# Kernel optimization log

Hardware: AMD Instinct MI355X
Metric: run time of the kernel (lower is better)

The kernel has to match this reference:

```python
import jax, jax.numpy as jnp
import numpy as np

HEADS = 16
HEAD_DIM = 64

def setup_inputs() -> dict:
    key = jax.random.key(0)
    ks = jax.random.split(key, 5)
    S, B, H = 1024, 4, 1024
    scale = 1.0 / np.sqrt(H)
    return {
        "hidden_states": jax.random.normal(ks[0], (S, B, H), jnp.float32),
        "attention_mask": jnp.zeros((B * HEADS, 1, S), jnp.float32),
        "Wq": jax.random.normal(ks[1], (H, H), jnp.float32) * scale,
        "bq": jnp.zeros((H,), jnp.float32),
        "Wk": jax.random.normal(ks[2], (H, H), jnp.float32) * scale,
        "bk": jnp.zeros((H,), jnp.float32),
        "Wv": jax.random.normal(ks[3], (H, H), jnp.float32) * scale,
        "bv": jnp.zeros((H,), jnp.float32),
    }

def reference(hidden_states, attention_mask, Wq, bq, Wk, bk, Wv, bv):
    S, B, H = hidden_states.shape
    d = HEAD_DIM
    inv_sqrt_d = 1.0 / np.sqrt(d)
    # QKV projections (torch Linear: x @ W.T + b)
    q = hidden_states @ Wq.T + bq  # (S, B, H)
    k = hidden_states @ Wk.T + bk
    v = hidden_states @ Wv.T + bv
    # (S, B*heads, d) -> (B*heads, S, d)
    q = q.reshape(S, B * HEADS, d).transpose(1, 0, 2)
    k = k.reshape(S, B * HEADS, d).transpose(1, 0, 2)
    v = v.reshape(S, B * HEADS, d).transpose(1, 0, 2)
    # SDDMM: scaled scores + additive mask -> (B*heads, S, S)
    scores = jnp.einsum('nsd,ntd->nst', q, k) * inv_sqrt_d + attention_mask
    probs = jax.nn.softmax(scores, axis=-1)
    # AV bmm -> (B*heads, S, d); note: dropout in source is seeded but never applied
    ctx = jnp.einsum('nst,ntd->nsd', probs, v)
    # back to (S, B, hidden)
    ctx = ctx.transpose(1, 0, 2).reshape(S, B, H)
    return ctx
```

## Files before the change

### kernel.cpp

```cpp
#include <hip/hip_runtime.h>
#include <hip/hip_bf16.h>
#include <math.h>

#define S_LEN 1024
#define BATCH 4
#define HID 1024
#define NHEADS 16
#define DHEAD 64
#define NTOT 64
#define M_ROWS 4096

typedef unsigned short u16;
typedef unsigned int u32;
typedef __bf16 bf16x8 __attribute__((ext_vector_type(8)));
typedef float f32x4 __attribute__((ext_vector_type(4)));

__device__ __forceinline__ u16 f2bf(float x) {
    __hip_bfloat16 h = __float2bfloat16(x);
    return *(u16*)&h;
}

__device__ __forceinline__ void gll16(const u16* g, u16* l) {
    __builtin_amdgcn_global_load_lds(
        (const __attribute__((address_space(1))) u32*)g,
        (__attribute__((address_space(3))) u32*)l, 16, 0, 0);
}

__global__ __launch_bounds__(256) void cvt_all(
    const float* __restrict__ X, const float* __restrict__ wq,
    const float* __restrict__ wk, const float* __restrict__ wv,
    u16* __restrict__ Xb, u16* __restrict__ Wb)
{
    const int bid = blockIdx.x;
    const float* src;
    u16* dst;
    size_t base;
    if (bid < 4096) {
        src = X; dst = Xb; base = (size_t)bid * 1024;
    } else {
        const int wb = bid - 4096;
        const int which = wb >> 10;
        src = (which == 0) ? wq : (which == 1) ? wk : wv;
        dst = Wb + (size_t)which * HID * HID;
        base = (size_t)(wb & 1023) * 1024;
    }
    const size_t idx = base + threadIdx.x * 4;
    float4 x = *(const float4*)(src + (bid < 4096 ? idx : (size_t)(idx - base) + base - ((bid < 4096) ? 0 : 0)));
    x = *(const float4*)(src + ((bid < 4096) ? idx : (base - base) + idx - ((size_t)0)));
    x = *(const float4*)(src + ((bid < 4096) ? idx : (idx - (size_t)0) - ((bid < 4096) ? 0 : (size_t)0)));
    x = *(const float4*)(src + (bid < 4096 ? idx : idx - (size_t)0 - 0));
    const size_t loc = (bid < 4096) ? idx : base + threadIdx.x * 4;
    x = *(const float4*)(src + loc);
    *(ushort4*)(dst + loc) = make_ushort4(f2bf(x.x), f2bf(x.y), f2bf(x.z), f2bf(x.w));
}

__global__ __launch_bounds__(256, 3) void qkv_mfma(
    const u16* __restrict__ Xb, const u16* __restrict__ Wb,
    const float* __restrict__ bq, const float* __restrict__ bk,
    const float* __restrict__ bv,
    u16* __restrict__ Qb, u16* __restrict__ Kb, u16* __restrict__ VT)
{
    const int m0 = blockIdx.x * 128;
    const int n0 = blockIdx.y * 128;
    const int which = blockIdx.z;

    __shared__ __align__(16) u16 As[128 * 32];
    __shared__ __align__(16) u16 Bs[128 * 32];

    const int tid = threadIdx.x;
    const int lane = tid & 63;
    const int w = tid >> 6;
    const int wm = w & 1, wn = w >> 1;
    const int quad = lane >> 4;
    const int l15 = lane & 15;

    const u16* W = Wb + (size_t)which * HID * HID;

    f32x4 acc[4][4];
    #pragma unroll
    for (int i = 0; i < 4; ++i)
        #pragma unroll
        for (int j = 0; j < 4; ++j)
            #pragma unroll
            for (int r = 0; r < 4; ++r) acc[i][j][r] = 0.0f;

    const int lrow = lane >> 2, lchk = (lane & 3) * 8;

    for (int k0 = 0; k0 < HID; k0 += 32) {
        #pragma unroll
        for (int c = 0; c < 2; ++c) {
            const int seg = w * 2 + c;
            const int row = seg * 16 + lrow;
            gll16(Xb + (size_t)(m0 + row) * HID + k0 + lchk, As + seg * 512);
            gll16(W  + (size_t)(n0 + row) * HID + k0 + lchk, Bs + seg * 512);
        }
        __syncthreads();

        bf16x8 af[4], bf[4];
        #pragma unroll
        for (int i = 0; i < 4; ++i)
            af[i] = *(const bf16x8*)(As + (wm * 64 + i * 16 + l15) * 32 + quad * 8);
        #pragma unroll
        for (int j = 0; j < 4; ++j)
            bf[j] = *(const bf16x8*)(Bs + (wn * 64 + j * 16 + l15) * 32 + quad * 8);
        #pragma unroll
        for (int i = 0; i < 4; ++i)
            #pragma unroll
            for (int j = 0; j < 4; ++j)
                acc[i][j] = __builtin_amdgcn_mfma_f32_16x16x32_bf16(
                    af[i], bf[j], acc[i][j], 0, 0, 0);
        __syncthreads();
    }

    const float* bias = (which == 0) ? bq : (which == 1) ? bk : bv;
    #pragma unroll
    for (int j = 0; j < 4; ++j) {
        const int o = n0 + wn * 64 + j * 16 + l15;
        const float bias_v = bias[o];
        const int head = o >> 6, d = o & 63;
        #pragma unroll
        for (int i = 0; i < 4; ++i) {
            const int mbase = m0 + wm * 64 + i * 16 + quad * 4;
            const int s = mbase >> 2;
            #pragma unroll
            for (int r = 0; r < 4; ++r) {
                const int n = r * NHEADS + head;
                const u16 hv = f2bf(acc[i][j][r] + bias_v);
                if (which == 0)
                    Qb[((size_t)n * S_LEN + s) * DHEAD + d] = hv;
                else if (which == 1)
                    Kb[((size_t)n * S_LEN + s) * DHEAD + d] = hv;
                else
                    VT[(size_t)n * (DHEAD * S_LEN) + (size_t)d * S_LEN + s] = hv;
            }
        }
    }
}

__global__ __launch_bounds__(256, 2) void attn_mfma(
    const u16* __restrict__ Qb, const u16* __restrict__ Kb,
    const u16* __restrict__ VT, const float* __restrict__ mask,
    float* __restrict__ out)
{
    const int n = blockIdx.y;
    const int s0 = blockIdx.x * 128;
    const int b = n >> 4, head = n & 15;

    __shared__ __align__(16) u16 Kbuf[2][64 * 64];
    __shared__ __align__(16) u16 Vbuf[2][64 * 64];
    __shared__ __align__(16) u16 Ps[128 * 64];

    const int tid = threadIdx.x;
    const int lane = tid & 63;
    const int w = tid >> 6;
    const int quad = lane >> 4;
    const int l15 = lane & 15;
    const size_t nbase = (size_t)n * S_LEN * DHEAD;

    int xs0 = ((quad ^ (l15 & 7)) * 8);
    int xs1 = (((4 + quad) ^ (l15 & 7)) * 8);

    const int srow = lane >> 3;
    const int scg  = (lane & 7) ^ (srow & 7);

    bf16x8 qf[2][2];
    #pragma unroll
    for (int mi = 0; mi < 2; ++mi)
        #pragma unroll
        for (int st = 0; st < 2; ++st)
            qf[mi][st] = *(const bf16x8*)(Qb + nbase +
                (size_t)(s0 + w * 32 + mi * 16 + l15) * 64 + st * 32 + quad * 8);

    f32x4 O[2][4];
    float l_part[2][4];
    #pragma unroll
    for (int mi = 0; mi < 2; ++mi)
        #pragma unroll
        for (int r = 0; r < 4; ++r) {
            l_part[mi][r] = 0.0f;
            #pragma unroll
            for (int jt = 0; jt < 4; ++jt) O[mi][jt][r] = 0.0f;
        }

    {
        const u16* Kg = Kb + nbase;
        const u16* Vg = VT + nbase;
        #pragma unroll
        for (int c = 0; c < 2; ++c) {
            const int seg = w * 2 + c;
            const int row = seg * 8 + srow;
            gll16(Kg + (size_t)row * 64 + scg * 8, Kbuf[0] + seg * 512);
            gll16(Vg + (size_t)row * S_LEN + scg * 8, Vbuf[0] + seg * 512);
        }
    }
    __syncthreads();

    for (int it = 0; it < 16; ++it) {
        const int t0 = it * 64;
        const u16* kb = Kbuf[it & 1];
        const u16* vb = Vbuf[it & 1];

        if (it < 15) {
            const u16* Kg = Kb + nbase + (size_t)(t0 + 64) * 64;
            const u16* Vg = VT + nbase + (t0 + 64);
            u16* kd = Kbuf[(it + 1) & 1];
            u16* vd = Vbuf[(it + 1) & 1];
            #pragma unroll
            for (int c = 0; c < 2; ++c) {
                const int seg = w * 2 + c;
                const int row = seg * 8 + srow;
                gll16(Kg + (size_t)row * 64 + scg * 8, kd + seg * 512);
                gll16(Vg + (size_t)row * S_LEN + scg * 8, vd + seg * 512);
            }
        }

        f32x4 sc[2][4];
        #pragma unroll
        for (int mi = 0; mi < 2; ++mi)
            #pragma unroll
            for (int j = 0; j < 4; ++j)
                #pragma unroll
                for (int r = 0; r < 4; ++r) sc[mi][j][r] = 0.0f;

        #pragma unroll
        for (int st = 0; st < 2; ++st) {
            const int xo = st ? xs1 : xs0;
            bf16x8 kf[4];
            #pragma unroll
            for (int j = 0; j < 4; ++j)
                kf[j] = *(const bf16x8*)(kb + (j * 16 + l15) * 64 + xo);
            #pragma unroll
            for (int mi = 0; mi < 2; ++mi)
                #pragma unroll
                for (int j = 0; j < 4; ++j)
                    sc[mi][j] = __builtin_amdgcn_mfma_f32_16x16x32_bf16(
                        qf[mi][st], kf[j], sc[mi][j], 0, 0, 0);
        }

        float mvm[4];
        #pragma unroll
        for (int j = 0; j < 4; ++j)
            mvm[j] = mask[(size_t)n * S_LEN + t0 + j * 16 + l15] - 16.0f;

        #pragma unroll
        for (int mi = 0; mi < 2; ++mi)
            #pragma unroll
            for (int r = 0; r < 4; ++r) {
                const int q = w * 32 + mi * 16 + quad * 4 + r;
                const int q7 = (quad * 4 + r) & 7;
                #pragma unroll
                for (int j = 0; j < 4; ++j) {
                    const float p = __expf(fmaf(sc[mi][j][r], 0.125f, mvm[j]));
                    l_part[mi][r] += p;
                    const int clog = j * 2 + (l15 >> 3);
                    Ps[q * 64 + (clog ^ q7) * 8 + (l15 & 7)] = f2bf(p);
                }
            }

        #pragma unroll
        for (int st = 0; st < 2; ++st) {
            const int xo = st ? xs1 : xs0;
            bf16x8 vf[4];
            #pragma unroll
            for (int jt = 0; jt < 4; ++jt)
                vf[jt] = *(const bf16x8*)(vb + (jt * 16 + l15) * 64 + xo);
            #pragma unroll
            for (int mi = 0; mi < 2; ++mi) {
                bf16x8 pf = *(const bf16x8*)(Ps + (w * 32 + mi * 16 + l15) * 64 + xo);
                #pragma unroll
                for (int jt = 0; jt < 4; ++jt)
                    O[mi][jt] = __builtin_amdgcn_mfma_f32_16x16x32_bf16(
                        pf, vf[jt], O[mi][jt], 0, 0, 0);
            }
        }

        __syncthreads();
    }

    #pragma unroll
    for (int mi = 0; mi < 2; ++mi)
        #pragma unroll
        for (int r = 0; r < 4; ++r) {
            float lr = l_part[mi][r];
            #pragma unroll
            for (int off = 8; off >= 1; off >>= 1) lr += __shfl_xor(lr, off);
            const float inv_l = 1.0f / lr;
            const int s = s0 + w * 32 + mi * 16 + quad * 4 + r;
            #pragma unroll
            for (int jt = 0; jt < 4; ++jt) {
                const int d = jt * 16 + l15;
                out[(size_t)s * (BATCH * HID) + (size_t)b * HID + head * DHEAD + d] =
                    O[mi][jt][r] * inv_l;
            }
        }
}

extern "C" void kernel_launch(void* const* d_in, const int* in_sizes, int n_in,
                              void* d_out, int out_size, void* d_ws, size_t ws_size,
                              hipStream_t stream)
{
    const float* X    = (const float*)d_in[0];
    const float* mask = (const float*)d_in[1];
    const float* Wq   = (const float*)d_in[2];
    const float* bq   = (const float*)d_in[3];
    const float* Wk   = (const float*)d_in[4];
    const float* bk   = (const float*)d_in[5];
    const float* Wv   = (const float*)d_in[6];
    const float* bv   = (const float*)d_in[7];
    float* out = (float*)d_out;

    const size_t MX = (size_t)M_ROWS * HID;
    const size_t MW = (size_t)HID * HID;
    u16* wsp = (u16*)d_ws;
    u16* Xb = wsp;
    u16* Wb = Xb + MX;
    u16* Qb = Wb + 3 * MW;
    u16* Kb = Qb + MX;
    u16* VT = Kb + MX;

    cvt_all<<<dim3(4096 + 3072), 256, 0, stream>>>(X, Wq, Wk, Wv, Xb, Wb);
    qkv_mfma<<<dim3(M_ROWS / 128, HID / 128, 3), 256, 0, stream>>>(
        Xb, Wb, bq, bk, bv, Qb, Kb, VT);
    attn_mfma<<<dim3(S_LEN / 128, NTOT), 256, 0, stream>>>(Qb, Kb, VT, mask, out);
}
```

Before: 166.0 us.

## Transpose MFMA operands in attention, pad P tile, stage output through LDS

Swaps the A/B operands of both MFMA chains so each lane holds four consecutive key columns per query row. This makes the mask load a float4 and the P write into LDS a packed ushort4 into a 72-wide padded tile instead of scattered scalar bf16 stores. Row sums now reduce with two cross-lane shuffles. The output is normalized, staged through reused LDS and written with coalesced float4 global stores. It also removes the redundant repeated loads in the conversion kernel. LDS use per block grows slightly, to 51200 bytes, which could limit occupancy.

After: 158.9 us. 1.04x faster.

```diff
diff --git a/kernel.cpp b/kernel.cpp
--- a/kernel.cpp
+++ b/kernel.cpp
@@ -34,24 +34,19 @@
     const int bid = blockIdx.x;
     const float* src;
     u16* dst;
-    size_t base;
+    size_t off;
     if (bid < 4096) {
-        src = X; dst = Xb; base = (size_t)bid * 1024;
+        src = X; dst = Xb; off = (size_t)bid * 1024;
     } else {
         const int wb = bid - 4096;
         const int which = wb >> 10;
         src = (which == 0) ? wq : (which == 1) ? wk : wv;
         dst = Wb + (size_t)which * HID * HID;
-        base = (size_t)(wb & 1023) * 1024;
-    }
-    const size_t idx = base + threadIdx.x * 4;
-    float4 x = *(const float4*)(src + (bid < 4096 ? idx : (size_t)(idx - base) + base - ((bid < 4096) ? 0 : 0)));
-    x = *(const float4*)(src + ((bid < 4096) ? idx : (base - base) + idx - ((size_t)0)));
-    x = *(const float4*)(src + ((bid < 4096) ? idx : (idx - (size_t)0) - ((bid < 4096) ? 0 : (size_t)0)));
-    x = *(const float4*)(src + (bid < 4096 ? idx : idx - (size_t)0 - 0));
-    const size_t loc = (bid < 4096) ? idx : base + threadIdx.x * 4;
-    x = *(const float4*)(src + loc);
-    *(ushort4*)(dst + loc) = make_ushort4(f2bf(x.x), f2bf(x.y), f2bf(x.z), f2bf(x.w));
+        off = (size_t)(wb & 1023) * 1024;
+    }
+    const size_t idx = off + threadIdx.x * 4;
+    float4 x = *(const float4*)(src + idx);
+    *(ushort4*)(dst + idx) = make_ushort4(f2bf(x.x), f2bf(x.y), f2bf(x.z), f2bf(x.w));
 }
 
 __global__ __launch_bounds__(256, 3) void qkv_mfma(
@@ -146,9 +141,11 @@
     const int s0 = blockIdx.x * 128;
     const int b = n >> 4, head = n & 15;
 
-    __shared__ __align__(16) u16 Kbuf[2][64 * 64];
-    __shared__ __align__(16) u16 Vbuf[2][64 * 64];
-    __shared__ __align__(16) u16 Ps[128 * 64];
+    __shared__ __align__(16) char smem[51200];
+    u16* Kbuf = (u16*)smem;
+    u16* Vbuf = (u16*)(smem + 16384);
+    u16* Ps   = (u16*)(smem + 32768);
+    float* Of = (float*)smem;
 
     const int tid = threadIdx.x;
     const int lane = tid & 63;
@@ -157,8 +154,8 @@
     const int l15 = lane & 15;
     const size_t nbase = (size_t)n * S_LEN * DHEAD;
 
-    int xs0 = ((quad ^ (l15 & 7)) * 8);
-    int xs1 = (((4 + quad) ^ (l15 & 7)) * 8);
+    const int xs0 = ((quad ^ (l15 & 7)) * 8);
+    const int xs1 = (((4 + quad) ^ (l15 & 7)) * 8);
 
     const int srow = lane >> 3;
     const int scg  = (lane & 7) ^ (srow & 7);
@@ -172,45 +169,41 @@
                 (size_t)(s0 + w * 32 + mi * 16 + l15) * 64 + st * 32 + quad * 8);
 
     f32x4 O[2][4];
-    float l_part[2][4];
-    #pragma unroll
-    for (int mi = 0; mi < 2; ++mi)
-        #pragma unroll
-        for (int r = 0; r < 4; ++r) {
-            l_part[mi][r] = 0.0f;
-            #pragma unroll
-            for (int jt = 0; jt < 4; ++jt) O[mi][jt][r] = 0.0f;
-        }
+    float l_lane[2];
+    #pragma unroll
+    for (int mi = 0; mi < 2; ++mi) {
+        l_lane[mi] = 0.0f;
+        #pragma unroll
+        for (int jt = 0; jt < 4; ++jt)
+            #pragma unroll
+            for (int r = 0; r < 4; ++r) O[mi][jt][r] = 0.0f;
+    }
 
     {
-        const u16* Kg = Kb + nbase;
-        const u16* Vg = VT + nbase;
         #pragma unroll
         for (int c = 0; c < 2; ++c) {
             const int seg = w * 2 + c;
             const int row = seg * 8 + srow;
-            gll16(Kg + (size_t)row * 64 + scg * 8, Kbuf[0] + seg * 512);
-            gll16(Vg + (size_t)row * S_LEN + scg * 8, Vbuf[0] + seg * 512);
+            gll16(Kb + nbase + (size_t)row * 64 + scg * 8, Kbuf + seg * 512);
+            gll16(VT + nbase + (size_t)row * S_LEN + scg * 8, Vbuf + seg * 512);
         }
     }
     __syncthreads();
 
     for (int it = 0; it < 16; ++it) {
         const int t0 = it * 64;
-        const u16* kb = Kbuf[it & 1];
-        const u16* vb = Vbuf[it & 1];
+        const u16* kb = Kbuf + (it & 1) * 4096;
+        const u16* vb = Vbuf + (it & 1) * 4096;
 
         if (it < 15) {
-            const u16* Kg = Kb + nbase + (size_t)(t0 + 64) * 64;
-            const u16* Vg = VT + nbase + (t0 + 64);
-            u16* kd = Kbuf[(it + 1) & 1];
-            u16* vd = Vbuf[(it + 1) & 1];
+            u16* kd = Kbuf + ((it + 1) & 1) * 4096;
+            u16* vd = Vbuf + ((it + 1) & 1) * 4096;
             #pragma unroll
             for (int c = 0; c < 2; ++c) {
                 const int seg = w * 2 + c;
                 const int row = seg * 8 + srow;
-                gll16(Kg + (size_t)row * 64 + scg * 8, kd + seg * 512);
-                gll16(Vg + (size_t)row * S_LEN + scg * 8, vd + seg * 512);
+                gll16(Kb + nbase + (size_t)(t0 + 64 + row) * 64 + scg * 8, kd + seg * 512);
+                gll16(VT + nbase + (size_t)row * S_LEN + t0 + 64 + scg * 8, vd + seg * 512);
             }
         }
 
@@ -234,28 +227,28 @@
                 #pragma unroll
                 for (int j = 0; j < 4; ++j)
                     sc[mi][j] = __builtin_amdgcn_mfma_f32_16x16x32_bf16(
-                        qf[mi][st], kf[j], sc[mi][j], 0, 0, 0);
-        }
-
-        float mvm[4];
+                        kf[j], qf[mi][st], sc[mi][j], 0, 0, 0);
+        }
+
+        float4 mv4[4];
         #pragma unroll
         for (int j = 0; j < 4; ++j)
-            mvm[j] = mask[(size_t)n * S_LEN + t0 + j * 16 + l15] - 16.0f;
-
-        #pragma unroll
-        for (int mi = 0; mi < 2; ++mi)
-            #pragma unroll
-            for (int r = 0; r < 4; ++r) {
-                const int q = w * 32 + mi * 16 + quad * 4 + r;
-                const int q7 = (quad * 4 + r) & 7;
-                #pragma unroll
-                for (int j = 0; j < 4; ++j) {
-                    const float p = __expf(fmaf(sc[mi][j][r], 0.125f, mvm[j]));
-                    l_part[mi][r] += p;
-                    const int clog = j * 2 + (l15 >> 3);
-                    Ps[q * 64 + (clog ^ q7) * 8 + (l15 & 7)] = f2bf(p);
-                }
+            mv4[j] = *(const float4*)(mask + (size_t)n * S_LEN + t0 + j * 16 + quad * 4);
+
+        #pragma unroll
+        for (int mi = 0; mi < 2; ++mi) {
+            const int q = w * 32 + mi * 16 + l15;
+            #pragma unroll
+            for (int j = 0; j < 4; ++j) {
+                const float p0 = __expf(fmaf(sc[mi][j][0], 0.125f, mv4[j].x - 16.0f));
+                const float p1 = __expf(fmaf(sc[mi][j][1], 0.125f, mv4[j].y - 16.0f));
+                const float p2 = __expf(fmaf(sc[mi][j][2], 0.125f, mv4[j].z - 16.0f));
+                const float p3 = __expf(fmaf(sc[mi][j][3], 0.125f, mv4[j].w - 16.0f));
+                l_lane[mi] += (p0 + p1) + (p2 + p3);
+                *(ushort4*)(Ps + q * 72 + j * 16 + quad * 4) =
+                    make_ushort4(f2bf(p0), f2bf(p1), f2bf(p2), f2bf(p3));
             }
+        }
 
         #pragma unroll
         for (int st = 0; st < 2; ++st) {
@@ -266,33 +259,47 @@
                 vf[jt] = *(const bf16x8*)(vb + (jt * 16 + l15) * 64 + xo);
             #pragma unroll
             for (int mi = 0; mi < 2; ++mi) {
-                bf16x8 pf = *(const bf16x8*)(Ps + (w * 32 + mi * 16 + l15) * 64 + xo);
+                bf16x8 pf = *(const bf16x8*)(Ps + (w * 32 + mi * 16 + l15) * 72 +
+                                             st * 32 + quad * 8);
                 #pragma unroll
                 for (int jt = 0; jt < 4; ++jt)
                     O[mi][jt] = __builtin_amdgcn_mfma_f32_16x16x32_bf16(
-                        pf, vf[jt], O[mi][jt], 0, 0, 0);
+                        vf[jt], pf, O[mi][jt], 0, 0, 0);
             }
         }
 
         __syncthreads();
     }
 
-    #pragma unroll
-    for (int mi = 0; mi < 2; ++mi)
-        #pragma unroll
-        for (int r = 0; r < 4; ++r) {
-            float lr = l_part[mi][r];
-            #pragma unroll
-            for (int off = 8; off >= 1; off >>= 1) lr += __shfl_xor(lr, off);
-            const float inv_l = 1.0f / lr;
-            const int s = s0 + w * 32 + mi * 16 + quad * 4 + r;
-            #pragma unroll
-            for (int jt = 0; jt < 4; ++jt) {
-                const int d = jt * 16 + l15;
-                out[(size_t)s * (BATCH * HID) + (size_t)b * HID + head * DHEAD + d] =
-                    O[mi][jt][r] * inv_l;
-            }
-        }
+    float inv_l[2];
+    #pragma unroll
+    for (int mi = 0; mi < 2; ++mi) {
+        float l = l_lane[mi];
+        l += __shfl_xor(l, 16);
+        l += __shfl_xor(l, 32);
+        inv_l[mi] = 1.0f / l;
+    }
+    __syncthreads();
+
+    #pragma unroll
+    for (int mi = 0; mi < 2; ++mi) {
+        const int q = w * 32 + mi * 16 + l15;
+        #pragma unroll
+        for (int jt = 0; jt < 4; ++jt)
+            #pragma unroll
+            for (int r = 0; r < 4; ++r)
+                Of[q * 72 + jt * 16 + quad * 4 + r] = O[mi][jt][r] * inv_l[mi];
+    }
+    __syncthreads();
+
+    const int tx = tid & 15, ty = tid >> 4;
+    #pragma unroll
+    for (int p = 0; p < 8; ++p) {
+        const int q = p * 16 + ty;
+        float4 v = *(const float4*)(Of + q * 72 + tx * 4);
+        *(float4*)(out + (size_t)(s0 + q) * (BATCH * HID) + (size_t)b * HID +
+                   head * DHEAD + tx * 4) = v;
+    }
 }
 
 extern "C" void kernel_launch(void* const* d_in, const int* in_sizes, int n_in,
```
